# Optimization experiments

Measured on AMD Instinct MI355X. Metric: run time of the kernel, lower is better.

Reference implementation:

```python
import jax, jax.numpy as jnp
import numpy as np

N_IN, D_IN, N_OUT, D_OUT = 1152, 8, 10, 16
ROUTINGS, NUM_BG = 3, 1
C, H, W = 1, 28, 28
BATCH = 128
DEC_IN = N_OUT * D_OUT  # 160, projection_type=None -> dec_feature_size = outcaps_size


def squash(x, axis=-1):
    norm = jnp.linalg.norm(x, axis=axis, keepdims=True)
    scale = norm ** 2 / (1.0 + norm ** 2) / (norm + 1e-8)
    return scale * x


def scale_coef(x, num_bg):
    # x: [B, n_out] or [B, n_out, n_in]; min/max normalize over dim 1,
    # excluding the last num_bg (background) capsules, then floor at 0.5.
    if num_bg > 0:
        xm = x[:, : x.shape[1] - num_bg]
    else:
        xm = x
    mn = jnp.min(xm, axis=1, keepdims=True)
    mx = jnp.max(xm, axis=1, keepdims=True)
    out = (xm - mn) / jnp.maximum(mx - mn, 1e-6)  # vrange (0,1)
    if num_bg > 0:
        out = jnp.concatenate([out, jnp.zeros_like(out[:, :num_bg])], axis=1)
    return jnp.maximum(out, 0.5)


def decode(capsflat, W1, b1, W2, b2, W3, b3):
    # fcn decoder (eval mode: dropout is identity): 160 -> 512 -> 1024 -> C*H*W
    h = jax.nn.relu(capsflat @ W1 + b1)
    h = jax.nn.relu(h @ W2 + b2)
    return jax.nn.sigmoid(h @ W3 + b3)


def setup_inputs() -> dict:
    key = jax.random.key(0)
    ks = jax.random.split(key, 9)
    return {
        'incaps': jax.random.normal(ks[0], (BATCH, N_IN, D_IN), jnp.float32),
        'x_input': jax.random.uniform(ks[1], (BATCH, C, H, W), jnp.float32),
        'weight': 0.1 * jax.random.normal(ks[2], (N_OUT, N_IN, D_OUT, D_IN), jnp.float32),
        'W1': 0.05 * jax.random.normal(ks[3], (DEC_IN, 512), jnp.float32),
        'b1': jnp.zeros((512,), jnp.float32),
        'W2': 0.05 * jax.random.normal(ks[4], (512, 1024), jnp.float32),
        'b2': jnp.zeros((1024,), jnp.float32),
        'W3': 0.05 * jax.random.normal(ks[5], (1024, C * H * W), jnp.float32),
        'b3': jnp.zeros((C * H * W,), jnp.float32),
    }


def reference(incaps, x_input, weight, W1, b1, W2, b2, W3, b3):
    B = incaps.shape[0]
    # outcaps_hat: matmul(weight, incaps[:,None,:,:,None]).squeeze(-1)
    hat = jnp.einsum('nkoi,bki->bnko', weight, incaps)  # [B, n_out, n_in, d_out]
    hat_d = jax.lax.stop_gradient(hat)
    rc = jnp.ones((B, N_OUT, N_IN), hat.dtype)
    eye = jnp.eye(N_OUT, dtype=hat.dtype)
    x_flat = x_input.reshape(B, 1, -1)
    for _ in range(ROUTINGS - 1):
        # squash over capsule dim, weighted sum over input capsules
        outcaps = squash(jnp.sum(rc[..., None] * hat_d, axis=2, keepdims=True))  # [B,n,1,d]
        b = jnp.sum(outcaps * hat_d, axis=-1)  # agreement [B, n_out, n_in]
        c = scale_coef(b, NUM_BG)
        objcaps = outcaps[:, :, 0, :]  # [B, n_out, d_out]
        # get_every_obj_rscore vectorized: mask one object capsule at a time
        masked = objcaps[:, None, :, :] * eye[None, :, :, None]  # [B, n_obj, n_out, d]
        recon = decode(masked.reshape(B, N_OUT, DEC_IN), W1, b1, W2, b2, W3, b3)  # [B,n_obj,CHW]
        rscore = -jnp.sum((x_flat - recon) ** 2, axis=-1)  # neg MSE-sum, [B, n_obj]
        r = scale_coef(rscore, NUM_BG)
        rc = c * r[:, :, None]
    # final iteration uses non-detached hat
    outcaps = squash(jnp.sum(rc[..., None] * hat, axis=2, keepdims=True))
    return outcaps[:, :, 0, :]  # [B, n_out, d_out]
```

## Files before the change

### kernel.cpp

```cpp
#include <hip/hip_runtime.h>
#include <math.h>

#define BATCH  128
#define NIN    1152
#define DIN    8
#define NOUTC  10
#define DOUT   16
#define H1DIM  512
#define H2DIM  1024
#define PIX    784
#define NROWS  (BATCH * NOUTC)
#define MROWS  (BATCH * 9)
#define NBY3   13

typedef __attribute__((ext_vector_type(8))) __bf16 bf16x8;
typedef __attribute__((ext_vector_type(4))) float  f32x4;
typedef __attribute__((ext_vector_type(4))) unsigned int u32x4;

__device__ __forceinline__ float bf2f(unsigned int u) {
    union { unsigned int i; float f; } v; v.i = u << 16; return v.f;
}
__device__ __forceinline__ ushort f2bf(float f) {
    union { float f; unsigned int i; } v; v.f = f;
    unsigned int r = v.i + 0x7FFFu + ((v.i >> 16) & 1u);
    return (ushort)(r >> 16);
}
__device__ __forceinline__ float ldin(const void* p, size_t i, int isbf) {
    return isbf ? bf2f(((const ushort*)p)[i]) : ((const float*)p)[i];
}
__device__ __forceinline__ bf16x8 frag_of(uint4 u) {
    return __builtin_bit_cast(bf16x8, u);
}
__device__ __forceinline__ bf16x8 ld_frag(const ushort* p) {
    return frag_of(*(const uint4*)p);
}
__device__ __forceinline__ float dot8(uint4 a, uint4 b) {
    float s;
    s  = bf2f(a.x & 0xffffu) * bf2f(b.x & 0xffffu);
    s += bf2f(a.x >> 16)     * bf2f(b.x >> 16);
    s += bf2f(a.y & 0xffffu) * bf2f(b.y & 0xffffu);
    s += bf2f(a.y >> 16)     * bf2f(b.y >> 16);
    s += bf2f(a.z & 0xffffu) * bf2f(b.z & 0xffffu);
    s += bf2f(a.z >> 16)     * bf2f(b.z >> 16);
    s += bf2f(a.w & 0xffffu) * bf2f(b.w & 0xffffu);
    s += bf2f(a.w >> 16)     * bf2f(b.w >> 16);
    return s;
}
__device__ __forceinline__ uint4 pack8(float4 a, float4 b) {
    uint4 r;
    r.x = f2bf(a.x) | ((unsigned)f2bf(a.y) << 16);
    r.y = f2bf(a.z) | ((unsigned)f2bf(a.w) << 16);
    r.z = f2bf(b.x) | ((unsigned)f2bf(b.y) << 16);
    r.w = f2bf(b.z) | ((unsigned)f2bf(b.w) << 16);
    return r;
}
__device__ __forceinline__ int detect_bf(const void* w, int* cntS) {
    int tid = threadIdx.x, nt = blockDim.x;
    if (tid == 0) *cntS = 0;
    __syncthreads();
    const ushort* u = (const ushort*)w;
    int c = 0;
    for (int s = tid; s < 512; s += nt) {
        int e = (u[s * 2] >> 7) & 0xFF;
        if (e >= 88 && e <= 140) c++;
    }
    atomicAdd(cntS, c);
    __syncthreads();
    return (*cntS >= 384) ? 1 : 0;
}

struct PrepArgs {
    const void* w;
    const void* inc;
    ushort*     hatG;
    const void* src[7];
    ushort*     dst[7];
    int         n[7];
    int*        flag;
};

__global__ __launch_bounds__(256) void prep_kernel(PrepArgs a)
{
    __shared__ int cntS;
    __shared__ ushort tile[32][33];
    int tid = threadIdx.x;
    int isbf = detect_bf(a.w, &cntS);
    int seg = blockIdx.y;
    if (seg == 0 && blockIdx.x == 0 && tid == 0) *a.flag = isbf;

    if (seg <= 4) {
        int n = a.n[seg];
        int stride = gridDim.x * 256;
        ushort* d = a.dst[seg];
        if (isbf) {
            const ushort* s = (const ushort*)a.src[seg];
            for (int i = blockIdx.x * 256 + tid; i < n; i += stride) d[i] = s[i];
        } else {
            const float* s = (const float*)a.src[seg];
            for (int i = blockIdx.x * 256 + tid; i < n; i += stride) d[i] = f2bf(s[i]);
        }
        return;
    }
    if (seg == 7) {
        if (!a.hatG || blockIdx.x >= 720) return;
        int u = blockIdx.x;
        int kc = u % 9, r = u / 9, bc = r % 8, n = r / 8;
        int k = kc * 128 + (tid >> 1);
        int oh = (tid & 1) << 3;
        size_t wbase = ((size_t)n * NIN + k) * DOUT + oh;
        uint4 wr[8];
        if (isbf) {
            const uint4* wp = (const uint4*)((const ushort*)a.w + wbase * DIN);
            #pragma unroll
            for (int j = 0; j < 8; j++) wr[j] = wp[j];
        } else {
            const float4* wp = (const float4*)((const float*)a.w + wbase * DIN);
            #pragma unroll
            for (int j = 0; j < 8; j++) wr[j] = pack8(wp[2 * j], wp[2 * j + 1]);
        }
        int b0 = bc * 16;
        #pragma unroll 4
        for (int bl = 0; bl < 16; bl++) {
            int b = b0 + bl;
            size_t ioff = ((size_t)b * NIN + k) * DIN;
            uint4 iu;
            if (isbf) iu = *(const uint4*)((const ushort*)a.inc + ioff);
            else {
                const float4* ip = (const float4*)((const float*)a.inc + ioff);
                iu = pack8(ip[0], ip[1]);
            }
            unsigned int h[8];
            #pragma unroll
            for (int j = 0; j < 8; j++) h[j] = f2bf(dot8(wr[j], iu));
            u32x4 ov = { h[0] | (h[1] << 16), h[2] | (h[3] << 16),
                         h[4] | (h[5] << 16), h[6] | (h[7] << 16) };
            __builtin_nontemporal_store(ov,
                (u32x4*)(a.hatG + (((size_t)(b * NOUTC + n) * NIN + k) * DOUT + oh)));
        }
        return;
    }
    int R = (seg == 5) ? H1DIM : H2DIM;
    int C = (seg == 5) ? H2DIM : PIX;
    int tilesX = (seg == 5) ? 32 : 25;
    int tilesY = (seg == 5) ? 16 : 32;
    int t = blockIdx.x;
    if (t >= tilesX * tilesY) return;
    int tx2 = t % tilesX, ty2 = t / tilesX;
    int c0 = tx2 * 32, r0 = ty2 * 32;
    const void* in = a.src[seg];
    ushort* out = a.dst[seg];
    int tx = tid & 31, ty = tid >> 5;
    for (int i = ty; i < 32; i += 8) {
        int r = r0 + i, c = c0 + tx;
        tile[i][tx] = (r < R && c < C) ? f2bf(ldin(in, (size_t)r * C + c, isbf)) : (ushort)0;
    }
    __syncthreads();
    for (int i = ty; i < 32; i += 8) {
        int c = c0 + i, r = r0 + tx;
        if (c < C && r < R) out[(size_t)c * R + r] = tile[tx][i];
    }
}

template<bool COMPUTE>
__global__ __launch_bounds__(512, 4) void reduce_pass(
    const ushort* __restrict__ hatG,
    const void*   __restrict__ incRaw,
    const void*   __restrict__ wRaw,
    const ushort* __restrict__ cbuf,
    const float*  __restrict__ partials,
    int iter0,
    const ushort* __restrict__ W1c,
    const ushort* __restrict__ b1c,
    ushort* __restrict__ h1out,
    ushort* __restrict__ bsOut,
    void*   __restrict__ outFinal,
    const int* __restrict__ flagp)
{
    int bn  = blockIdx.x;
    int n   = bn % NOUTC;
    int b   = bn / NOUTC;
    int tid = threadIdx.x;

    __shared__ ushort wSb[NIN];
    __shared__ float  redS[8][16];
    __shared__ float  sumS[16];
    __shared__ float  ocS[16];
    __shared__ float  scaleS;

    int h = tid & 1, kb = tid >> 1;
    int wave = tid >> 6, lane = tid & 63;

    uint4 v[4];
    const ushort* tailS;

    if constexpr (!COMPUTE) {
        __shared__ uint4 hatTail4[256];
        const ushort* hbase = hatG + (size_t)bn * NIN * DOUT;
        #pragma unroll
        for (int j = 0; j < 4; j++)
            v[j] = *(const uint4*)(hbase + ((kb + 256 * j) * DOUT + h * 8));
        if (tid < 256)
            hatTail4[tid] = *(const uint4*)(hbase + 1024 * DOUT + tid * 8);
        tailS = (const ushort*)hatTail4;
    } else {
        __shared__ int cntS;
        __shared__ uint4 hatS4[NIN * DOUT / 8];
        int isbf = detect_bf(wRaw, &cntS);
        size_t wnb = (size_t)n * NIN * DOUT * DIN;
        for (int idx = tid; idx < NIN * DOUT; idx += 512) {
            int k = idx >> 4;
            float s = 0.f;
            #pragma unroll
            for (int i = 0; i < 8; i++)
                s += ldin(wRaw, wnb + (size_t)idx * 8 + i, isbf) *
                     ldin(incRaw, ((size_t)b * NIN + k) * DIN + i, isbf);
            ((ushort*)hatS4)[idx] = f2bf(s);
        }
        __syncthreads();
        const ushort* hbase = (const ushort*)hatS4;
        #pragma unroll
        for (int j = 0; j < 4; j++)
            v[j] = *(const uint4*)(hbase + ((kb + 256 * j) * DOUT + h * 8));
        tailS = hbase + 1024 * DOUT;
    }

    if (!iter0) {
        if (tid < 9) {
            float s = 0.f;
            #pragma unroll
            for (int j = 0; j < NBY3; j++)
                s += partials[(size_t)(b * 9 + tid) * 16 + j];
            sumS[tid] = -s;
        }
        __syncthreads();
        float mn = 1e30f, mx = -1e30f;
        #pragma unroll
        for (int n2 = 0; n2 < 9; n2++) {
            float vv = sumS[n2];
            mn = fminf(mn, vv); mx = fmaxf(mx, vv);
        }
        float den = fmaxf(mx - mn, 1e-6f);
        float rv = (n < 9) ? fmaxf((sumS[n] - mn) / den, 0.5f) : 0.5f;
        const ushort* crow = cbuf + (size_t)bn * NIN;
        for (int k = tid; k < NIN; k += 512)
            wSb[k] = f2bf(bf2f(crow[k]) * rv);
    }
    __syncthreads();

    float acc[8];
    #pragma unroll
    for (int o = 0; o < 8; o++) acc[o] = 0.f;
    #pragma unroll
    for (int j = 0; j < 4; j++) {
        int k = kb + 256 * j;
        float w = iter0 ? 1.f : bf2f(wSb[k]);
        bf16x8 hv = frag_of(v[j]);
        #pragma unroll
        for (int o = 0; o < 8; o++) acc[o] += w * (float)hv[o];
    }
    if (tid < 256) {
        int k = 1024 + kb;
        float w = iter0 ? 1.f : bf2f(wSb[k]);
        bf16x8 hv = ld_frag(tailS + kb * DOUT + h * 8);
        #pragma unroll
        for (int o = 0; o < 8; o++) acc[o] += w * (float)hv[o];
    }
    #pragma unroll
    for (int off = 32; off >= 2; off >>= 1) {
        #pragma unroll
        for (int o = 0; o < 8; o++) acc[o] += __shfl_xor(acc[o], off);
    }
    if (lane < 2) {
        #pragma unroll
        for (int o = 0; o < 8; o++) redS[wave][lane * 8 + o] = acc[o];
    }
    __syncthreads();
    if (tid < 16) {
        float s = 0.f;
        #pragma unroll
        for (int wv = 0; wv < 8; wv++) s += redS[wv][tid];
        sumS[tid] = s;
    }
    __syncthreads();
    if (tid == 0) {
        float n2 = 0.f;
        #pragma unroll
        for (int o = 0; o < 16; o++) n2 += sumS[o] * sumS[o];
        float nrm = sqrtf(n2);
        scaleS = n2 / (1.f + n2) / (nrm + 1e-8f);
    }
    __syncthreads();
    if (tid < 16) {
        float oc = scaleS * sumS[tid];
        ocS[tid] = oc;
        if (outFinal) {
            if (*flagp) ((ushort*)outFinal)[(size_t)bn * 16 + tid] = f2bf(oc);
            else        ((float*) outFinal)[(size_t)bn * 16 + tid] = oc;
        }
    }
    __syncthreads();

    if (bsOut && n < 9) {
        float o0 = ocS[h * 8 + 0], o1 = ocS[h * 8 + 1], o2 = ocS[h * 8 + 2],
              o3 = ocS[h * 8 + 3], o4 = ocS[h * 8 + 4], o5 = ocS[h * 8 + 5],
              o6 = ocS[h * 8 + 6], o7 = ocS[h * 8 + 7];
        #pragma unroll
        for (int j = 0; j < 4; j++) {
            bf16x8 hv = frag_of(v[j]);
            float s = o0 * (float)hv[0] + o1 * (float)hv[1] + o2 * (float)hv[2] +
                      o3 * (float)hv[3] + o4 * (float)hv[4] + o5 * (float)hv[5] +
                      o6 * (float)hv[6] + o7 * (float)hv[7];
            s += __shfl_xor(s, 1);
            if (h == 0) bsOut[(size_t)bn * NIN + kb + 256 * j] = f2bf(s);
        }
        if (tid < 256) {
            bf16x8 hv = ld_frag(tailS + kb * DOUT + h * 8);
            float s = o0 * (float)hv[0] + o1 * (float)hv[1] + o2 * (float)hv[2] +
                      o3 * (float)hv[3] + o4 * (float)hv[4] + o5 * (float)hv[5] +
                      o6 * (float)hv[6] + o7 * (float)hv[7];
            s += __shfl_xor(s, 1);
            if (h == 0) bsOut[(size_t)bn * NIN + 1024 + kb] = f2bf(s);
        }
    }

    if (h1out && n < 9) {
        int col = tid;
        float acc1 = bf2f(b1c[col]);
        #pragma unroll
        for (int i = 0; i < 16; i++)
            acc1 += ocS[i] * bf2f(W1c[(size_t)(n * 16 + i) * H1DIM + col]);
        h1out[(size_t)(b * 9 + n) * H1DIM + col] = f2bf(fmaxf(acc1, 0.f));
    }
}

__global__ __launch_bounds__(256) void gemm2_kernel(
    const ushort* __restrict__ A, const ushort* __restrict__ Bt,
    const ushort* __restrict__ bias, ushort* __restrict__ Cout,
    const ushort* __restrict__ bs, ushort* __restrict__ cbuf)
{
    if (blockIdx.y >= 16) {
        int ci = (blockIdx.y - 16) * 18 + blockIdx.x;
        int base = ci * 4096 + threadIdx.x;
        #pragma unroll 4
        for (int j = 0; j < 16; j++) {
            int pi = base + j * 256;
            int b = pi / NIN, k = pi - b * NIN;
            const ushort* bp = bs + (size_t)b * NOUTC * NIN + k;
            float vv[9], mn = 1e30f, mx = -1e30f;
            #pragma unroll
            for (int n2 = 0; n2 < 9; n2++) {
                vv[n2] = bf2f(bp[n2 * NIN]);
                mn = fminf(mn, vv[n2]); mx = fmaxf(mx, vv[n2]);
            }
            float den = fmaxf(mx - mn, 1e-6f);
            ushort* cp = cbuf + (size_t)b * NOUTC * NIN + k;
            #pragma unroll
            for (int n2 = 0; n2 < 9; n2++)
                cp[n2 * NIN] = f2bf(fmaxf((vv[n2] - mn) / den, 0.5f));
            cp[9 * NIN] = f2bf(0.5f);
        }
        return;
    }
    int m0 = blockIdx.x * 64, n0 = blockIdx.y * 64;
    int tid = threadIdx.x;
    int wave = tid >> 6, lane = tid & 63, quad = lane >> 4, l16 = lane & 15;

    __shared__ uint4 As4[320];
    __shared__ uint4 Bs4[320];
    ushort* As = (ushort*)As4;
    ushort* Bs = (ushort*)Bs4;

    f32x4 acc[4];
    #pragma unroll
    for (int nt = 0; nt < 4; nt++)
        #pragma unroll
        for (int rg = 0; rg < 4; rg++) acc[nt][rg] = 0.f;

    int sMi = tid >> 2, sKk = (tid & 3) * 8;
    int sLds = sMi * 5 + (tid & 3);
    const ushort* Ap = A + (size_t)(m0 + sMi) * H1DIM + sKk;
    const ushort* Bp = Bt + (size_t)(n0 + sMi) * H1DIM + sKk;

    uint4 aR = *(const uint4*)Ap;
    uint4 bR = *(const uint4*)Bp;

    for (int k0 = 0; k0 < H1DIM; k0 += 32) {
        As4[sLds] = aR;
        Bs4[sLds] = bR;
        __syncthreads();
        if (k0 + 32 < H1DIM) {
            aR = *(const uint4*)(Ap + k0 + 32);
            bR = *(const uint4*)(Bp + k0 + 32);
        }
        bf16x8 a = ld_frag(As + (wave * 16 + l16) * 40 + quad * 8);
        #pragma unroll
        for (int nt = 0; nt < 4; nt++) {
            bf16x8 bb = ld_frag(Bs + (nt * 16 + l16) * 40 + quad * 8);
            acc[nt] = __builtin_amdgcn_mfma_f32_16x16x32_bf16(a, bb, acc[nt], 0, 0, 0);
        }
        __syncthreads();
    }

    int rowBase = m0 + wave * 16 + quad * 4;
    #pragma unroll
    for (int nt = 0; nt < 4; nt++) {
        int col = n0 + nt * 16 + l16;
        float bv = bf2f(bias[col]);
        #pragma unroll
        for (int rg = 0; rg < 4; rg++) {
            float v = acc[nt][rg] + bv;
            Cout[(size_t)(rowBase + rg) * H2DIM + col] = f2bf(fmaxf(v, 0.f));
        }
    }
}

__global__ __launch_bounds__(256) void gemm3_kernel(
    const ushort* __restrict__ A, const ushort* __restrict__ Bt,
    const ushort* __restrict__ bias,
    const ushort* __restrict__ xin, float* __restrict__ partials)
{
    int m0 = blockIdx.x * 64, n0 = blockIdx.y * 64;
    int tid = threadIdx.x;
    int wave = tid >> 6, lane = tid & 63, quad = lane >> 4, l16 = lane & 15;

    __shared__ uint4 As4[320];
    __shared__ uint4 Bs4[320];
    ushort* As = (ushort*)As4;
    ushort* Bs = (ushort*)Bs4;

    f32x4 acc[4];
    #pragma unroll
    for (int nt = 0; nt < 4; nt++)
        #pragma unroll
        for (int rg = 0; rg < 4; rg++) acc[nt][rg] = 0.f;

    int sMi = tid >> 2, sKk = (tid & 3) * 8;
    int sLds = sMi * 5 + (tid & 3);
    const ushort* Ap = A + (size_t)(m0 + sMi) * H2DIM + sKk;
    const ushort* Bp = Bt + (size_t)(n0 + sMi) * H2DIM + sKk;
    bool bOK = (n0 + sMi) < PIX;

    uint4 aR = *(const uint4*)Ap;
    uint4 bR = bOK ? *(const uint4*)Bp : make_uint4(0, 0, 0, 0);

    for (int k0 = 0; k0 < H2DIM; k0 += 32) {
        As4[sLds] = aR;
        Bs4[sLds] = bR;
        __syncthreads();
        if (k0 + 32 < H2DIM) {
            aR = *(const uint4*)(Ap + k0 + 32);
            bR = bOK ? *(const uint4*)(Bp + k0 + 32) : make_uint4(0, 0, 0, 0);
        }
        bf16x8 a = ld_frag(As + (wave * 16 + l16) * 40 + quad * 8);
        #pragma unroll
        for (int nt = 0; nt < 4; nt++) {
            bf16x8 bb = ld_frag(Bs + (nt * 16 + l16) * 40 + quad * 8);
            acc[nt] = __builtin_amdgcn_mfma_f32_16x16x32_bf16(a, bb, acc[nt], 0, 0, 0);
        }
        __syncthreads();
    }

    int rowBase = m0 + wave * 16 + quad * 4;
    float vr[4] = {0.f, 0.f, 0.f, 0.f};
    #pragma unroll
    for (int nt = 0; nt < 4; nt++) {
        int col = n0 + nt * 16 + l16;
        if (col < PIX) {
            float bv = bf2f(bias[col]);
            #pragma unroll
            for (int rg = 0; rg < 4; rg++) {
                int row = rowBase + rg;
                int bb = row / 9;
                float z = acc[nt][rg] + bv;
                float s = 1.f / (1.f + __expf(-z));
                float d = bf2f(xin[(size_t)bb * PIX + col]) - s;
                vr[rg] += d * d;
            }
        }
    }
    #pragma unroll
    for (int rg = 0; rg < 4; rg++) {
        float v = vr[rg];
        #pragma unroll
        for (int off = 8; off >= 1; off >>= 1) v += __shfl_xor(v, off, 16);
        if (l16 == 0)
            partials[(size_t)(rowBase + rg) * 16 + blockIdx.y] = v;
    }
}

extern "C" void kernel_launch(void* const* d_in, const int* in_sizes, int n_in,
                              void* d_out, int out_size, void* d_ws, size_t ws_size,
                              hipStream_t stream)
{
    const void* inc = d_in[0];
    const void* x   = d_in[1];
    const void* w   = d_in[2];
    const void* W1  = d_in[3];
    const void* b1  = d_in[4];
    const void* W2  = d_in[5];
    const void* b2  = d_in[6];
    const void* W3  = d_in[7];
    const void* b3  = d_in[8];

    char* p = (char*)d_ws;
    auto alloc = [&](size_t bytes) { void* r = p; p += (bytes + 255) & ~(size_t)255; return r; };
    int*    flagWS    = (int*)alloc(256);
    ushort* bs        = (ushort*)alloc((size_t)NROWS * NIN * 2);
    ushort* cbuf      = (ushort*)alloc((size_t)NROWS * NIN * 2);
    float*  partials  = (float*)alloc((size_t)MROWS * 16 * 4);
    ushort* h1WS      = (ushort*)alloc((size_t)MROWS * H1DIM * 2);
    ushort* h2WS      = (ushort*)alloc((size_t)MROWS * H2DIM * 2);
    ushort* W2T       = (ushort*)alloc((size_t)H2DIM * H1DIM * 2);
    ushort* W3T       = (ushort*)alloc((size_t)PIX * H2DIM * 2);
    ushort* W1c       = (ushort*)alloc((size_t)160 * H1DIM * 2);
    ushort* b1c       = (ushort*)alloc((size_t)H1DIM * 2);
    ushort* b2c       = (ushort*)alloc((size_t)H2DIM * 2);
    ushort* b3c       = (ushort*)alloc((size_t)PIX * 2);
    ushort* xc        = (ushort*)alloc((size_t)BATCH * PIX * 2);
    ushort* hatG      = (ushort*)alloc((size_t)NROWS * NIN * DOUT * 2);
    bool haveHat = ((char*)hatG + (size_t)NROWS * NIN * DOUT * 2) <= ((char*)d_ws + ws_size);

    PrepArgs pa;
    pa.w = w; pa.inc = inc; pa.hatG = haveHat ? hatG : nullptr;
    pa.src[0] = W1;  pa.dst[0] = W1c;  pa.n[0] = 160 * H1DIM;
    pa.src[1] = b1;  pa.dst[1] = b1c;  pa.n[1] = H1DIM;
    pa.src[2] = b2;  pa.dst[2] = b2c;  pa.n[2] = H2DIM;
    pa.src[3] = b3;  pa.dst[3] = b3c;  pa.n[3] = PIX;
    pa.src[4] = x;   pa.dst[4] = xc;   pa.n[4] = BATCH * PIX;
    pa.src[5] = W2;  pa.dst[5] = W2T;  pa.n[5] = 0;
    pa.src[6] = W3;  pa.dst[6] = W3T;  pa.n[6] = 0;
    pa.flag = flagWS;
    prep_kernel<<<dim3(800, 8), 256, 0, stream>>>(pa);

    if (haveHat)
        reduce_pass<false><<<NROWS, 512, 0, stream>>>(
            hatG, inc, w, nullptr, nullptr, 1,
            W1c, b1c, h1WS, bs, nullptr, flagWS);
    else
        reduce_pass<true><<<NROWS, 512, 0, stream>>>(
            nullptr, inc, w, nullptr, nullptr, 1,
            W1c, b1c, h1WS, bs, nullptr, flagWS);

    for (int it = 0; it < 2; it++) {
        gemm2_kernel<<<dim3(18, 18), 256, 0, stream>>>(
            h1WS, W2T, b2c, h2WS, bs, cbuf);
        gemm3_kernel<<<dim3(18, NBY3), 256, 0, stream>>>(
            h2WS, W3T, b3c, xc, partials);

        int last = (it == 1);
        ushort* bsO = last ? nullptr : bs;
        ushort* h1o = last ? nullptr : h1WS;
        void*   fin = last ? d_out : nullptr;
        if (haveHat)
            reduce_pass<false><<<NROWS, 512, 0, stream>>>(
                hatG, inc, w, cbuf, partials, 0,
                W1c, b1c, h1o, bsO, fin, flagWS);
        else
            reduce_pass<true><<<NROWS, 512, 0, stream>>>(
                nullptr, inc, w, cbuf, partials, 0,
                W1c, b1c, h1o, bsO, fin, flagWS);
    }
}
```

Baseline: 217.7 us.

## Recompute capsule predictions in-register instead of materializing hat tensor in global memory

Removes the precompute stage that wrote the full per-batch prediction tensor to a workspace buffer, and has each routing reduce pass recompute its predictions from weight and input capsules in registers. The intent is to trade a large global write and three large re-reads for redundant dot-product compute and weight reads that should hit in cache. It also drops the shared-memory tail staging and the fallback path, and reads the precision flag once per block.

```diff
diff --git a/kernel.cpp b/kernel.cpp
--- a/kernel.cpp
+++ b/kernel.cpp
@@ -15,7 +15,6 @@
 
 typedef __attribute__((ext_vector_type(8))) __bf16 bf16x8;
 typedef __attribute__((ext_vector_type(4))) float  f32x4;
-typedef __attribute__((ext_vector_type(4))) unsigned int u32x4;
 
 __device__ __forceinline__ float bf2f(unsigned int u) {
     union { unsigned int i; float f; } v; v.i = u << 16; return v.f;
@@ -71,8 +70,6 @@
 
 struct PrepArgs {
     const void* w;
-    const void* inc;
-    ushort*     hatG;
     const void* src[7];
     ushort*     dst[7];
     int         n[7];
@@ -98,44 +95,6 @@
         } else {
             const float* s = (const float*)a.src[seg];
             for (int i = blockIdx.x * 256 + tid; i < n; i += stride) d[i] = f2bf(s[i]);
-        }
-        return;
-    }
-    if (seg == 7) {
-        if (!a.hatG || blockIdx.x >= 720) return;
-        int u = blockIdx.x;
-        int kc = u % 9, r = u / 9, bc = r % 8, n = r / 8;
-        int k = kc * 128 + (tid >> 1);
-        int oh = (tid & 1) << 3;
-        size_t wbase = ((size_t)n * NIN + k) * DOUT + oh;
-        uint4 wr[8];
-        if (isbf) {
-            const uint4* wp = (const uint4*)((const ushort*)a.w + wbase * DIN);
-            #pragma unroll
-            for (int j = 0; j < 8; j++) wr[j] = wp[j];
-        } else {
-            const float4* wp = (const float4*)((const float*)a.w + wbase * DIN);
-            #pragma unroll
-            for (int j = 0; j < 8; j++) wr[j] = pack8(wp[2 * j], wp[2 * j + 1]);
-        }
-        int b0 = bc * 16;
-        #pragma unroll 4
-        for (int bl = 0; bl < 16; bl++) {
-            int b = b0 + bl;
-            size_t ioff = ((size_t)b * NIN + k) * DIN;
-            uint4 iu;
-            if (isbf) iu = *(const uint4*)((const ushort*)a.inc + ioff);
-            else {
-                const float4* ip = (const float4*)((const float*)a.inc + ioff);
-                iu = pack8(ip[0], ip[1]);
-            }
-            unsigned int h[8];
-            #pragma unroll
-            for (int j = 0; j < 8; j++) h[j] = f2bf(dot8(wr[j], iu));
-            u32x4 ov = { h[0] | (h[1] << 16), h[2] | (h[3] << 16),
-                         h[4] | (h[5] << 16), h[6] | (h[7] << 16) };
-            __builtin_nontemporal_store(ov,
-                (u32x4*)(a.hatG + (((size_t)(b * NOUTC + n) * NIN + k) * DOUT + oh)));
         }
         return;
     }
@@ -161,9 +120,7 @@
     }
 }
 
-template<bool COMPUTE>
 __global__ __launch_bounds__(512, 4) void reduce_pass(
-    const ushort* __restrict__ hatG,
     const void*   __restrict__ incRaw,
     const void*   __restrict__ wRaw,
     const ushort* __restrict__ cbuf,
@@ -180,6 +137,7 @@
     int n   = bn % NOUTC;
     int b   = bn / NOUTC;
     int tid = threadIdx.x;
+    int isbf = *flagp;
 
     __shared__ ushort wSb[NIN];
     __shared__ float  redS[8][16];
@@ -189,39 +147,33 @@
 
     int h = tid & 1, kb = tid >> 1;
     int wave = tid >> 6, lane = tid & 63;
-
-    uint4 v[4];
-    const ushort* tailS;
-
-    if constexpr (!COMPUTE) {
-        __shared__ uint4 hatTail4[256];
-        const ushort* hbase = hatG + (size_t)bn * NIN * DOUT;
-        #pragma unroll
-        for (int j = 0; j < 4; j++)
-            v[j] = *(const uint4*)(hbase + ((kb + 256 * j) * DOUT + h * 8));
-        if (tid < 256)
-            hatTail4[tid] = *(const uint4*)(hbase + 1024 * DOUT + tid * 8);
-        tailS = (const ushort*)hatTail4;
-    } else {
-        __shared__ int cntS;
-        __shared__ uint4 hatS4[NIN * DOUT / 8];
-        int isbf = detect_bf(wRaw, &cntS);
-        size_t wnb = (size_t)n * NIN * DOUT * DIN;
-        for (int idx = tid; idx < NIN * DOUT; idx += 512) {
-            int k = idx >> 4;
-            float s = 0.f;
-            #pragma unroll
-            for (int i = 0; i < 8; i++)
-                s += ldin(wRaw, wnb + (size_t)idx * 8 + i, isbf) *
-                     ldin(incRaw, ((size_t)b * NIN + k) * DIN + i, isbf);
-            ((ushort*)hatS4)[idx] = f2bf(s);
-        }
-        __syncthreads();
-        const ushort* hbase = (const ushort*)hatS4;
-        #pragma unroll
-        for (int j = 0; j < 4; j++)
-            v[j] = *(const uint4*)(hbase + ((kb + 256 * j) * DOUT + h * 8));
-        tailS = hbase + 1024 * DOUT;
+    int nrows = (tid < 256) ? 5 : 4;
+
+    uint4 v[5];
+    #pragma unroll
+    for (int j = 0; j < 5; j++) {
+        if (j >= nrows) break;
+        int k = kb + 256 * j;
+        size_t woff = ((size_t)n * NIN + k) * DOUT + (size_t)h * 8;
+        size_t ioff = ((size_t)b * NIN + k) * DIN;
+        uint4 iu;
+        unsigned int hh[8];
+        if (isbf) {
+            iu = *(const uint4*)((const ushort*)incRaw + ioff);
+            const uint4* wp = (const uint4*)((const ushort*)wRaw + woff * DIN);
+            #pragma unroll
+            for (int o = 0; o < 8; o++) hh[o] = f2bf(dot8(wp[o], iu));
+        } else {
+            const float4* ip = (const float4*)((const float*)incRaw + ioff);
+            iu = pack8(ip[0], ip[1]);
+            const float4* wp = (const float4*)((const float*)wRaw + woff * DIN);
+            #pragma unroll
+            for (int o = 0; o < 8; o++) hh[o] = f2bf(dot8(pack8(wp[2 * o], wp[2 * o + 1]), iu));
+        }
+        v[j].x = hh[0] | (hh[1] << 16);
+        v[j].y = hh[2] | (hh[3] << 16);
+        v[j].z = hh[4] | (hh[5] << 16);
+        v[j].w = hh[6] | (hh[7] << 16);
     }
 
     if (!iter0) {
@@ -251,17 +203,11 @@
     #pragma unroll
     for (int o = 0; o < 8; o++) acc[o] = 0.f;
     #pragma unroll
-    for (int j = 0; j < 4; j++) {
+    for (int j = 0; j < 5; j++) {
+        if (j >= nrows) break;
         int k = kb + 256 * j;
         float w = iter0 ? 1.f : bf2f(wSb[k]);
         bf16x8 hv = frag_of(v[j]);
-        #pragma unroll
-        for (int o = 0; o < 8; o++) acc[o] += w * (float)hv[o];
-    }
-    if (tid < 256) {
-        int k = 1024 + kb;
-        float w = iter0 ? 1.f : bf2f(wSb[k]);
-        bf16x8 hv = ld_frag(tailS + kb * DOUT + h * 8);
         #pragma unroll
         for (int o = 0; o < 8; o++) acc[o] += w * (float)hv[o];
     }
@@ -294,8 +240,8 @@
         float oc = scaleS * sumS[tid];
         ocS[tid] = oc;
         if (outFinal) {
-            if (*flagp) ((ushort*)outFinal)[(size_t)bn * 16 + tid] = f2bf(oc);
-            else        ((float*) outFinal)[(size_t)bn * 16 + tid] = oc;
+            if (isbf) ((ushort*)outFinal)[(size_t)bn * 16 + tid] = f2bf(oc);
+            else      ((float*) outFinal)[(size_t)bn * 16 + tid] = oc;
         }
     }
     __syncthreads();
@@ -305,21 +251,14 @@
               o3 = ocS[h * 8 + 3], o4 = ocS[h * 8 + 4], o5 = ocS[h * 8 + 5],
               o6 = ocS[h * 8 + 6], o7 = ocS[h * 8 + 7];
         #pragma unroll
-        for (int j = 0; j < 4; j++) {
+        for (int j = 0; j < 5; j++) {
+            if (j >= nrows) break;
             bf16x8 hv = frag_of(v[j]);
             float s = o0 * (float)hv[0] + o1 * (float)hv[1] + o2 * (float)hv[2] +
                       o3 * (float)hv[3] + o4 * (float)hv[4] + o5 * (float)hv[5] +
                       o6 * (float)hv[6] + o7 * (float)hv[7];
             s += __shfl_xor(s, 1);
             if (h == 0) bsOut[(size_t)bn * NIN + kb + 256 * j] = f2bf(s);
-        }
-        if (tid < 256) {
-            bf16x8 hv = ld_frag(tailS + kb * DOUT + h * 8);
-            float s = o0 * (float)hv[0] + o1 * (float)hv[1] + o2 * (float)hv[2] +
-                      o3 * (float)hv[3] + o4 * (float)hv[4] + o5 * (float)hv[5] +
-                      o6 * (float)hv[6] + o7 * (float)hv[7];
-            s += __shfl_xor(s, 1);
-            if (h == 0) bsOut[(size_t)bn * NIN + 1024 + kb] = f2bf(s);
         }
     }
 
@@ -517,11 +456,9 @@
     ushort* b2c       = (ushort*)alloc((size_t)H2DIM * 2);
     ushort* b3c       = (ushort*)alloc((size_t)PIX * 2);
     ushort* xc        = (ushort*)alloc((size_t)BATCH * PIX * 2);
-    ushort* hatG      = (ushort*)alloc((size_t)NROWS * NIN * DOUT * 2);
-    bool haveHat = ((char*)hatG + (size_t)NROWS * NIN * DOUT * 2) <= ((char*)d_ws + ws_size);
 
     PrepArgs pa;
-    pa.w = w; pa.inc = inc; pa.hatG = haveHat ? hatG : nullptr;
+    pa.w = w;
     pa.src[0] = W1;  pa.dst[0] = W1c;  pa.n[0] = 160 * H1DIM;
     pa.src[1] = b1;  pa.dst[1] = b1c;  pa.n[1] = H1DIM;
     pa.src[2] = b2;  pa.dst[2] = b2c;  pa.n[2] = H2DIM;
@@ -530,16 +467,11 @@
     pa.src[5] = W2;  pa.dst[5] = W2T;  pa.n[5] = 0;
     pa.src[6] = W3;  pa.dst[6] = W3T;  pa.n[6] = 0;
     pa.flag = flagWS;
-    prep_kernel<<<dim3(800, 8), 256, 0, stream>>>(pa);
-
-    if (haveHat)
-        reduce_pass<false><<<NROWS, 512, 0, stream>>>(
-            hatG, inc, w, nullptr, nullptr, 1,
-            W1c, b1c, h1WS, bs, nullptr, flagWS);
-    else
-        reduce_pass<true><<<NROWS, 512, 0, stream>>>(
-            nullptr, inc, w, nullptr, nullptr, 1,
-            W1c, b1c, h1WS, bs, nullptr, flagWS);
+    prep_kernel<<<dim3(800, 7), 256, 0, stream>>>(pa);
+
+    reduce_pass<<<NROWS, 512, 0, stream>>>(
+        inc, w, nullptr, nullptr, 1,
+        W1c, b1c, h1WS, bs, nullptr, flagWS);
 
     for (int it = 0; it < 2; it++) {
         gemm2_kernel<<<dim3(18, 18), 256, 0, stream>>>(
@@ -551,13 +483,8 @@
         ushort* bsO = last ? nullptr : bs;
         ushort* h1o = last ? nullptr : h1WS;
         void*   fin = last ? d_out : nullptr;
-        if (haveHat)
-            reduce_pass<false><<<NROWS, 512, 0, stream>>>(
-                hatG, inc, w, cbuf, partials, 0,
-                W1c, b1c, h1o, bsO, fin, flagWS);
-        else
-            reduce_pass<true><<<NROWS, 512, 0, stream>>>(
-                nullptr, inc, w, cbuf, partials, 0,
-                W1c, b1c, h1o, bsO, fin, flagWS);
-    }
-}
+        reduce_pass<<<NROWS, 512, 0, stream>>>(
+            inc, w, cbuf, partials, 0,
+            W1c, b1c, h1o, bsO, fin, flagWS);
+    }
+}
```

New measurement: 425.7 us. +95.5%, slower.
